# Performance work log

Hardware: AMD Instinct MI355X
Metric: run time of the kernel (lower is better)

Reference implementation:

```python
import jax, jax.numpy as jnp
import numpy as np

MEM_DIM = 2048
BATCH = 4096


def setup_inputs() -> dict:
    key = jax.random.key(0)
    ks = jax.random.split(key, 8)
    D = MEM_DIM
    scale = 1.0 / np.sqrt(D)  # torch nn.Linear default init range ~ U(-1/sqrt(D), 1/sqrt(D))
    lc = jax.random.normal(ks[0], (BATCH, D), dtype=jnp.float32)
    lh = jax.random.normal(ks[1], (BATCH, D), dtype=jnp.float32)
    rc = jax.random.normal(ks[2], (BATCH, D), dtype=jnp.float32)
    rh = jax.random.normal(ks[3], (BATCH, D), dtype=jnp.float32)
    # Fused params: columns [0:D]=input gate, [D:2D]=left forget, [2D:3D]=right forget, [3D:4D]=update
    Wl = jax.random.uniform(ks[4], (D, 4 * D), dtype=jnp.float32, minval=-scale, maxval=scale)
    Wr = jax.random.uniform(ks[5], (D, 4 * D), dtype=jnp.float32, minval=-scale, maxval=scale)
    bl = jax.random.uniform(ks[6], (4 * D,), dtype=jnp.float32, minval=-scale, maxval=scale)
    br = jax.random.uniform(ks[7], (4 * D,), dtype=jnp.float32, minval=-scale, maxval=scale)
    return {"lc": lc, "lh": lh, "rc": rc, "rh": rh, "Wl": Wl, "bl": bl, "Wr": Wr, "br": br}


def reference(lc, lh, rc, rh, Wl, bl, Wr, br):
    D = lh.shape[-1]
    # Two fused GEMMs replace 8 separate mem_dim x mem_dim linears (same math).
    g = jnp.dot(lh, Wl) + bl + jnp.dot(rh, Wr) + br  # [B, 4D]
    i = jax.nn.sigmoid(g[:, 0 * D:1 * D])   # input gate
    lf = jax.nn.sigmoid(g[:, 1 * D:2 * D])  # left forget gate
    rf = jax.nn.sigmoid(g[:, 2 * D:3 * D])  # right forget gate
    u = jnp.tanh(g[:, 3 * D:4 * D])         # cell update
    c = i * u + lf * lc + rf * rc
    h = jnp.tanh(c)
    return (c, h)
```

## Files before the change

### kernel.cpp

```cpp
#include <hip/hip_runtime.h>
#include <stdint.h>

#define D_MEM 2048
#define BATCH 4096
#define K_DIM 4096
#define N_DIM 8192

typedef __bf16 bf16x8 __attribute__((ext_vector_type(8)));
typedef float f32x4 __attribute__((ext_vector_type(4)));

typedef const void __attribute__((address_space(1)))* gas_t;
typedef void __attribute__((address_space(3)))* las_t;

__device__ __forceinline__ ushort f2b(float f) {
  union { float f; uint32_t u; } v; v.f = f;
  uint32_t u = v.u + 0x7fffu + ((v.u >> 16) & 1u);
  return (ushort)(u >> 16);
}
__device__ __forceinline__ float b2f(ushort s) {
  union { uint32_t u; float f; } v; v.u = ((uint32_t)s) << 16;
  return v.f;
}
__device__ __forceinline__ float sigm(float x) {
  return 1.0f / (1.0f + __expf(-x));
}
__device__ __forceinline__ float tanh_fast(float x) {
  return __builtin_fmaf(2.0f, sigm(2.0f * x), -1.0f);
}

__global__ void cast_concat_kernel(const float* __restrict__ lh,
                                   const float* __restrict__ rh,
                                   ushort* __restrict__ A) {
  int i4 = blockIdx.x * 256 + threadIdx.x;
  int row = i4 >> 10;
  int col = (i4 & 1023) * 4;
  const float* src = (col < D_MEM) ? (lh + (size_t)row * D_MEM + col)
                                   : (rh + (size_t)row * D_MEM + (col - D_MEM));
  float4 v = *(const float4*)src;
  ushort4 o; o.x = f2b(v.x); o.y = f2b(v.y); o.z = f2b(v.z); o.w = f2b(v.w);
  *(ushort4*)(A + (size_t)row * K_DIM + col) = o;
}

__global__ void transpose_cast_kernel(const float* __restrict__ Wl,
                                      const float* __restrict__ Wr,
                                      ushort* __restrict__ Bt) {
  __shared__ float t[64 * 65];
  const float* W = blockIdx.z ? Wr : Wl;
  int n0 = blockIdx.x * 64;
  int k0 = blockIdx.y * 64;
  int tid = threadIdx.x;
#pragma unroll
  for (int i = 0; i < 4; ++i) {
    int idx = i * 256 + tid;
    int rr = idx >> 4;
    int c4 = (idx & 15) * 4;
    float4 v = *(const float4*)(W + (size_t)(k0 + rr) * N_DIM + n0 + c4);
    t[rr * 65 + c4 + 0] = v.x;
    t[rr * 65 + c4 + 1] = v.y;
    t[rr * 65 + c4 + 2] = v.z;
    t[rr * 65 + c4 + 3] = v.w;
  }
  __syncthreads();
  int kbase = (blockIdx.z ? D_MEM : 0) + k0;
#pragma unroll
  for (int i = 0; i < 4; ++i) {
    int idx = i * 256 + tid;
    int rr = idx >> 4;
    int c4 = (idx & 15) * 4;
    ushort4 o;
    o.x = f2b(t[(c4 + 0) * 65 + rr]);
    o.y = f2b(t[(c4 + 1) * 65 + rr]);
    o.z = f2b(t[(c4 + 2) * 65 + rr]);
    o.w = f2b(t[(c4 + 3) * 65 + rr]);
    *(ushort4*)(Bt + (size_t)(n0 + rr) * K_DIM + kbase + c4) = o;
  }
}

__device__ __forceinline__ void stage2(const ushort* g0, const ushort* g1,
                                       char* dst, int wave) {
  __builtin_amdgcn_global_load_lds((gas_t)g0, (las_t)(dst + wave * 1024), 16, 0, 0);
  __builtin_amdgcn_global_load_lds((gas_t)g1, (las_t)(dst + 8192 + wave * 1024), 16, 0, 0);
}

#define HALF(KS, BUF, GA0, GA1, DSTA, GB0, GB1, DSTB)                          \
  do {                                                                         \
    stage2((GA0), (GA1), (DSTA), wave);                                        \
    stage2((GB0), (GB1), (DSTB), wave);                                        \
    bf16x8 af0[4], af1[4], bq[4];                                              \
    const char* ab_ = AsB + (BUF)*32768 + (KS)*16384;                          \
    const char* bb_ = BsB + (BUF)*32768 + (KS)*16384;                          \
    _Pragma("unroll") for (int f_ = 0; f_ < 4; ++f_)                           \
        af0[f_] = *(const bf16x8*)(ab_ + aoff[0][f_]);                         \
    _Pragma("unroll") for (int j_ = 0; j_ < 4; ++j_)                           \
        bq[j_] = *(const bf16x8*)(bb_ + boff[j_]);                             \
    _Pragma("unroll") for (int f_ = 0; f_ < 4; ++f_)                           \
        af1[f_] = *(const bf16x8*)(ab_ + aoff[1][f_]);                         \
    __builtin_amdgcn_s_setprio(1);                                             \
    _Pragma("unroll") for (int i_ = 0; i_ < 4; ++i_)                           \
        _Pragma("unroll") for (int j_ = 0; j_ < 4; ++j_)                       \
            acc[i_][j_] = __builtin_amdgcn_mfma_f32_16x16x32_bf16(             \
                af0[i_], bq[j_], acc[i_][j_], 0, 0, 0);                        \
    _Pragma("unroll") for (int i_ = 0; i_ < 4; ++i_)                           \
        _Pragma("unroll") for (int j_ = 0; j_ < 4; ++j_)                       \
            acc[4 + i_][j_] = __builtin_amdgcn_mfma_f32_16x16x32_bf16(         \
                af1[i_], bq[j_], acc[4 + i_][j_], 0, 0, 0);                    \
    __builtin_amdgcn_s_setprio(0);                                             \
    asm volatile("s_waitcnt vmcnt(8)" ::: "memory");                           \
    __builtin_amdgcn_s_barrier();                                              \
  } while (0)

__global__ __launch_bounds__(512, 2) void gemm_bf16_kernel(
    const ushort* __restrict__ A,
    const ushort* __restrict__ B,
    const float* __restrict__ bl,
    const float* __restrict__ br,
    const float* __restrict__ lc,
    const float* __restrict__ rc,
    float* __restrict__ out) {
  __shared__ char smem[131072];
  char* AsB = smem;
  char* BsB = smem + 65536;
  const int K = K_DIM;

  int tid = threadIdx.x;
  int lane = tid & 63, wave = tid >> 6;
  int wm = wave >> 2, wn = wave & 3;
  int q = lane >> 4, r = lane & 15;

  int bid = blockIdx.x;
  int swz = (bid & 7) * 64 + (bid >> 3);
  int m0 = (swz >> 5) * 256;
  int d0 = (swz & 31) * 64;

  int ci0 = tid, ci1 = 512 + tid;
  int r0 = ci0 >> 2, c0 = (ci0 & 3) ^ ((r0 ^ (r0 >> 2)) & 3);
  int r1 = ci1 >> 2, c1 = (ci1 & 3) ^ ((r1 ^ (r1 >> 2)) & 3);
  int nb0 = (r0 >> 6) * D_MEM + d0 + (r0 & 63);
  int nb1 = (r1 >> 6) * D_MEM + d0 + (r1 & 63);
  const ushort* sA0 = A + (size_t)(m0 + r0) * K + c0 * 8;
  const ushort* sA1 = A + (size_t)(m0 + r1) * K + c1 * 8;
  const ushort* sB0 = B + (size_t)nb0 * K + c0 * 8;
  const ushort* sB1 = B + (size_t)nb1 * K + c1 * 8;

  int swzr = (r ^ (r >> 2)) & 3;
  int aoff[2][4], boff[4];
#pragma unroll
  for (int mh = 0; mh < 2; ++mh)
#pragma unroll
    for (int f = 0; f < 4; ++f) {
      int row = wm * 128 + mh * 64 + f * 16 + r;
      aoff[mh][f] = row * 64 + (q ^ swzr) * 16;
    }
#pragma unroll
  for (int j = 0; j < 4; ++j) {
    int row = j * 64 + wn * 16 + r;
    boff[j] = row * 64 + (q ^ swzr) * 16;
  }

  f32x4 acc[8][4];
#pragma unroll
  for (int i = 0; i < 8; ++i)
#pragma unroll
    for (int j = 0; j < 4; ++j) acc[i][j] = f32x4{0.f, 0.f, 0.f, 0.f};

  stage2(sA0,      sA1,      AsB + 0,     wave);
  stage2(sB0,      sB1,      BsB + 0,     wave);
  stage2(sA0 + 32, sA1 + 32, AsB + 16384, wave);
  stage2(sB0 + 32, sB1 + 32, BsB + 16384, wave);
  stage2(sA0 + 64, sA1 + 64, AsB + 32768, wave);
  stage2(sB0 + 64, sB1 + 64, BsB + 32768, wave);
  asm volatile("s_waitcnt vmcnt(8)" ::: "memory");
  __builtin_amdgcn_s_barrier();

#pragma unroll 1
  for (int t = 0; t < 64; t += 2) {
    const int o1 = (t + 1) * 64;
    const int o2 = (t + 2 < 64 ? t + 2 : 63) * 64;
    const int o3 = (t + 3 < 64 ? t + 3 : 63) * 64;
    HALF(0, 0, sA0 + o1 + 32, sA1 + o1 + 32, AsB + 49152,
               sB0 + o1 + 32, sB1 + o1 + 32, BsB + 49152);
    HALF(1, 0, sA0 + o2,      sA1 + o2,      AsB + 0,
               sB0 + o2,      sB1 + o2,      BsB + 0);
    HALF(0, 1, sA0 + o2 + 32, sA1 + o2 + 32, AsB + 16384,
               sB0 + o2 + 32, sB1 + o2 + 32, BsB + 16384);
    HALF(1, 1, sA0 + o3,      sA1 + o3,      AsB + 32768,
               sB0 + o3,      sB1 + o3,      BsB + 32768);
  }

  int d = d0 + wn * 16 + r;
  float bs0 = bl[0 * D_MEM + d] + br[0 * D_MEM + d];
  float bs1 = bl[1 * D_MEM + d] + br[1 * D_MEM + d];
  float bs2 = bl[2 * D_MEM + d] + br[2 * D_MEM + d];
  float bs3 = bl[3 * D_MEM + d] + br[3 * D_MEM + d];
  float* outc = out + d;
  float* outh = out + (size_t)BATCH * D_MEM + d;

#pragma unroll
  for (int i = 0; i < 8; ++i) {
    int mb = m0 + wm * 128 + i * 16 + q * 4;
#pragma unroll
    for (int e = 0; e < 4; ++e) {
      size_t mrow = (size_t)(mb + e) * D_MEM;
      float gi = acc[i][0][e] + bs0;
      float gf = acc[i][1][e] + bs1;
      float gr = acc[i][2][e] + bs2;
      float gu = acc[i][3][e] + bs3;
      float c = sigm(gi) * tanh_fast(gu) + sigm(gf) * lc[mrow + d] +
                sigm(gr) * rc[mrow + d];
      outc[mrow] = c;
      outh[mrow] = tanh_fast(c);
    }
  }
}

extern "C" void kernel_launch(void* const* d_in, const int* in_sizes, int n_in,
                              void* d_out, int out_size, void* d_ws, size_t ws_size,
                              hipStream_t stream) {
  const float* lc = (const float*)d_in[0];
  const float* lh = (const float*)d_in[1];
  const float* rc = (const float*)d_in[2];
  const float* rh = (const float*)d_in[3];
  const float* Wl = (const float*)d_in[4];
  const float* bl = (const float*)d_in[5];
  const float* Wr = (const float*)d_in[6];
  const float* br = (const float*)d_in[7];
  float* out = (float*)d_out;

  char* ws = (char*)d_ws;
  ushort* A  = (ushort*)ws;
  ushort* Bt = (ushort*)(ws + (size_t)32 * 1024 * 1024);

  cast_concat_kernel<<<16384, 256, 0, stream>>>(lh, rh, A);
  dim3 tg(128, 32, 2);
  transpose_cast_kernel<<<tg, 256, 0, stream>>>(Wl, Wr, Bt);
  gemm_bf16_kernel<<<512, 512, 0, stream>>>(A, Bt, bl, br, lc, rc, out);
}
```

Measured before the change: 535.9 us.

## Use 16 waves per GEMM block with gate-interleaved weight layout

Doubles the GEMM block to 1024 threads, so each of 16 waves computes a 64x64 sub-tile instead of 8 waves computing 128x64. The transpose kernel now writes B rows interleaved per 16-column group (four gates adjacent), so one contiguous 256-row B tile is staged per block. Staging becomes one load per thread per stage into a four-slot rotating LDS ring. The aim is more waves per CU to hide latency. The cost is a lower MFMA-to-LDS-read ratio per wave, and the (1024,4) launch bounds may force a tight register cap that causes spills.

```diff
diff --git a/kernel.cpp b/kernel.cpp
--- a/kernel.cpp
+++ b/kernel.cpp
@@ -72,44 +72,15 @@
     o.y = f2b(t[(c4 + 1) * 65 + rr]);
     o.z = f2b(t[(c4 + 2) * 65 + rr]);
     o.w = f2b(t[(c4 + 3) * 65 + rr]);
-    *(ushort4*)(Bt + (size_t)(n0 + rr) * K_DIM + kbase + c4) = o;
-  }
-}
-
-__device__ __forceinline__ void stage2(const ushort* g0, const ushort* g1,
-                                       char* dst, int wave) {
-  __builtin_amdgcn_global_load_lds((gas_t)g0, (las_t)(dst + wave * 1024), 16, 0, 0);
-  __builtin_amdgcn_global_load_lds((gas_t)g1, (las_t)(dst + 8192 + wave * 1024), 16, 0, 0);
-}
-
-#define HALF(KS, BUF, GA0, GA1, DSTA, GB0, GB1, DSTB)                          \
-  do {                                                                         \
-    stage2((GA0), (GA1), (DSTA), wave);                                        \
-    stage2((GB0), (GB1), (DSTB), wave);                                        \
-    bf16x8 af0[4], af1[4], bq[4];                                              \
-    const char* ab_ = AsB + (BUF)*32768 + (KS)*16384;                          \
-    const char* bb_ = BsB + (BUF)*32768 + (KS)*16384;                          \
-    _Pragma("unroll") for (int f_ = 0; f_ < 4; ++f_)                           \
-        af0[f_] = *(const bf16x8*)(ab_ + aoff[0][f_]);                         \
-    _Pragma("unroll") for (int j_ = 0; j_ < 4; ++j_)                           \
-        bq[j_] = *(const bf16x8*)(bb_ + boff[j_]);                             \
-    _Pragma("unroll") for (int f_ = 0; f_ < 4; ++f_)                           \
-        af1[f_] = *(const bf16x8*)(ab_ + aoff[1][f_]);                         \
-    __builtin_amdgcn_s_setprio(1);                                             \
-    _Pragma("unroll") for (int i_ = 0; i_ < 4; ++i_)                           \
-        _Pragma("unroll") for (int j_ = 0; j_ < 4; ++j_)                       \
-            acc[i_][j_] = __builtin_amdgcn_mfma_f32_16x16x32_bf16(             \
-                af0[i_], bq[j_], acc[i_][j_], 0, 0, 0);                        \
-    _Pragma("unroll") for (int i_ = 0; i_ < 4; ++i_)                           \
-        _Pragma("unroll") for (int j_ = 0; j_ < 4; ++j_)                       \
-            acc[4 + i_][j_] = __builtin_amdgcn_mfma_f32_16x16x32_bf16(         \
-                af1[i_], bq[j_], acc[4 + i_][j_], 0, 0, 0);                    \
-    __builtin_amdgcn_s_setprio(0);                                             \
-    asm volatile("s_waitcnt vmcnt(8)" ::: "memory");                           \
-    __builtin_amdgcn_s_barrier();                                              \
-  } while (0)
-
-__global__ __launch_bounds__(512, 2) void gemm_bf16_kernel(
+    int n = n0 + rr;
+    int d = n & (D_MEM - 1);
+    int g = n >> 11;
+    int nrow = ((d >> 4) << 6) + (g << 4) + (d & 15);
+    *(ushort4*)(Bt + (size_t)nrow * K_DIM + kbase + c4) = o;
+  }
+}
+
+__global__ __launch_bounds__(1024, 4) void gemm_bf16_kernel(
     const ushort* __restrict__ A,
     const ushort* __restrict__ B,
     const float* __restrict__ bl,
@@ -132,60 +103,75 @@
   int m0 = (swz >> 5) * 256;
   int d0 = (swz & 31) * 64;
 
-  int ci0 = tid, ci1 = 512 + tid;
-  int r0 = ci0 >> 2, c0 = (ci0 & 3) ^ ((r0 ^ (r0 >> 2)) & 3);
-  int r1 = ci1 >> 2, c1 = (ci1 & 3) ^ ((r1 ^ (r1 >> 2)) & 3);
-  int nb0 = (r0 >> 6) * D_MEM + d0 + (r0 & 63);
-  int nb1 = (r1 >> 6) * D_MEM + d0 + (r1 & 63);
-  const ushort* sA0 = A + (size_t)(m0 + r0) * K + c0 * 8;
-  const ushort* sA1 = A + (size_t)(m0 + r1) * K + c1 * 8;
-  const ushort* sB0 = B + (size_t)nb0 * K + c0 * 8;
-  const ushort* sB1 = B + (size_t)nb1 * K + c1 * 8;
+  int sr = tid >> 2, sc = (tid & 3) ^ ((sr ^ (sr >> 2)) & 3);
+  const ushort* sA0 = A + (size_t)(m0 + sr) * K + sc * 8;
+  const ushort* sB0 = B + (size_t)(d0 * 4 + sr) * K + sc * 8;
 
   int swzr = (r ^ (r >> 2)) & 3;
-  int aoff[2][4], boff[4];
-#pragma unroll
-  for (int mh = 0; mh < 2; ++mh)
-#pragma unroll
-    for (int f = 0; f < 4; ++f) {
-      int row = wm * 128 + mh * 64 + f * 16 + r;
-      aoff[mh][f] = row * 64 + (q ^ swzr) * 16;
-    }
+  int aoff[4], boff[4];
+#pragma unroll
+  for (int f = 0; f < 4; ++f) {
+    int row = wm * 64 + f * 16 + r;
+    aoff[f] = row * 64 + (q ^ swzr) * 16;
+  }
 #pragma unroll
   for (int j = 0; j < 4; ++j) {
-    int row = j * 64 + wn * 16 + r;
-    boff[j] = row * 64 + (q ^ swzr) * 16;
-  }
-
-  f32x4 acc[8][4];
-#pragma unroll
-  for (int i = 0; i < 8; ++i)
+    int row = wn * 64 + j * 16 + r;
+    boff[j] = row * 64 + (q ^ ((row ^ (row >> 2)) & 3)) * 16;
+  }
+
+  f32x4 acc[4][4];
+#pragma unroll
+  for (int i = 0; i < 4; ++i)
 #pragma unroll
     for (int j = 0; j < 4; ++j) acc[i][j] = f32x4{0.f, 0.f, 0.f, 0.f};
 
-  stage2(sA0,      sA1,      AsB + 0,     wave);
-  stage2(sB0,      sB1,      BsB + 0,     wave);
-  stage2(sA0 + 32, sA1 + 32, AsB + 16384, wave);
-  stage2(sB0 + 32, sB1 + 32, BsB + 16384, wave);
-  stage2(sA0 + 64, sA1 + 64, AsB + 32768, wave);
-  stage2(sB0 + 64, sB1 + 64, BsB + 32768, wave);
-  asm volatile("s_waitcnt vmcnt(8)" ::: "memory");
+  int wb = wave * 1024;
+
+  __builtin_amdgcn_global_load_lds((gas_t)(sA0 +  0), (las_t)(AsB + 0     + wb), 16, 0, 0);
+  __builtin_amdgcn_global_load_lds((gas_t)(sB0 +  0), (las_t)(BsB + 0     + wb), 16, 0, 0);
+  __builtin_amdgcn_global_load_lds((gas_t)(sA0 + 32), (las_t)(AsB + 16384 + wb), 16, 0, 0);
+  __builtin_amdgcn_global_load_lds((gas_t)(sB0 + 32), (las_t)(BsB + 16384 + wb), 16, 0, 0);
+  __builtin_amdgcn_global_load_lds((gas_t)(sA0 + 64), (las_t)(AsB + 32768 + wb), 16, 0, 0);
+  __builtin_amdgcn_global_load_lds((gas_t)(sB0 + 64), (las_t)(BsB + 32768 + wb), 16, 0, 0);
+  asm volatile("s_waitcnt vmcnt(4)" ::: "memory");
   __builtin_amdgcn_s_barrier();
 
+#define HALF(P)                                                                \
+  do {                                                                         \
+    const int h_ = t2 + (P);                                                   \
+    const int rgn_ = (h_ & 3) * 16384;                                         \
+    const int sr_ = ((h_ + 3) & 3) * 16384;                                    \
+    const int so_ = (h_ + 3 < 128 ? h_ + 3 : 127) * 32;                        \
+    __builtin_amdgcn_global_load_lds((gas_t)(sA0 + so_),                       \
+                                     (las_t)(AsB + sr_ + wb), 16, 0, 0);       \
+    __builtin_amdgcn_global_load_lds((gas_t)(sB0 + so_),                       \
+                                     (las_t)(BsB + sr_ + wb), 16, 0, 0);       \
+    bf16x8 af[4], bq[4];                                                       \
+    const char* ab_ = AsB + rgn_;                                              \
+    const char* bb_ = BsB + rgn_;                                              \
+    _Pragma("unroll") for (int f_ = 0; f_ < 4; ++f_)                           \
+        af[f_] = *(const bf16x8*)(ab_ + aoff[f_]);                             \
+    _Pragma("unroll") for (int j_ = 0; j_ < 4; ++j_)                           \
+        bq[j_] = *(const bf16x8*)(bb_ + boff[j_]);                             \
+    __builtin_amdgcn_s_setprio(1);                                             \
+    _Pragma("unroll") for (int i_ = 0; i_ < 4; ++i_)                           \
+        _Pragma("unroll") for (int j_ = 0; j_ < 4; ++j_)                       \
+            acc[i_][j_] = __builtin_amdgcn_mfma_f32_16x16x32_bf16(             \
+                af[i_], bq[j_], acc[i_][j_], 0, 0, 0);                         \
+    __builtin_amdgcn_s_setprio(0);                                             \
+    asm volatile("s_waitcnt vmcnt(4)" ::: "memory");                           \
+    __builtin_amdgcn_s_barrier();                                              \
+  } while (0)
+
 #pragma unroll 1
-  for (int t = 0; t < 64; t += 2) {
-    const int o1 = (t + 1) * 64;
-    const int o2 = (t + 2 < 64 ? t + 2 : 63) * 64;
-    const int o3 = (t + 3 < 64 ? t + 3 : 63) * 64;
-    HALF(0, 0, sA0 + o1 + 32, sA1 + o1 + 32, AsB + 49152,
-               sB0 + o1 + 32, sB1 + o1 + 32, BsB + 49152);
-    HALF(1, 0, sA0 + o2,      sA1 + o2,      AsB + 0,
-               sB0 + o2,      sB1 + o2,      BsB + 0);
-    HALF(0, 1, sA0 + o2 + 32, sA1 + o2 + 32, AsB + 16384,
-               sB0 + o2 + 32, sB1 + o2 + 32, BsB + 16384);
-    HALF(1, 1, sA0 + o3,      sA1 + o3,      AsB + 32768,
-               sB0 + o3,      sB1 + o3,      BsB + 32768);
-  }
+  for (int t2 = 0; t2 < 128; t2 += 4) {
+    HALF(0);
+    HALF(1);
+    HALF(2);
+    HALF(3);
+  }
+#undef HALF
 
   int d = d0 + wn * 16 + r;
   float bs0 = bl[0 * D_MEM + d] + br[0 * D_MEM + d];
@@ -196,8 +182,8 @@
   float* outh = out + (size_t)BATCH * D_MEM + d;
 
 #pragma unroll
-  for (int i = 0; i < 8; ++i) {
-    int mb = m0 + wm * 128 + i * 16 + q * 4;
+  for (int i = 0; i < 4; ++i) {
+    int mb = m0 + wm * 64 + i * 16 + q * 4;
 #pragma unroll
     for (int e = 0; e < 4; ++e) {
       size_t mrow = (size_t)(mb + e) * D_MEM;
@@ -233,5 +219,5 @@
   cast_concat_kernel<<<16384, 256, 0, stream>>>(lh, rh, A);
   dim3 tg(128, 32, 2);
   transpose_cast_kernel<<<tg, 256, 0, stream>>>(Wl, Wr, Bt);
-  gemm_bf16_kernel<<<512, 512, 0, stream>>>(A, Bt, bl, br, lc, rc, out);
-}
+  gemm_bf16_kernel<<<512, 1024, 0, stream>>>(A, Bt, bl, br, lc, rc, out);
+}
```

Result: faster. 524.4 us (-2.2%).
